# Optimization experiments

Measured on AMD Instinct MI355X. Metric: run time of the kernel, lower is better.

The kernel has to match this reference:

```python
import jax, jax.numpy as jnp
import numpy as np

DIM = 384
H = 64
W = 64
NB = 8
BS = DIM // NB
WF = W // 2 + 1
EPS = 1e-5


def _layernorm(x, g, b):
    mu = jnp.mean(x, axis=-1, keepdims=True)
    var = jnp.mean(jnp.square(x - mu), axis=-1, keepdims=True)
    return (x - mu) * jax.lax.rsqrt(var + EPS) * g + b


def setup_inputs() -> dict:
    key = jax.random.key(0)
    ks = jax.random.split(key, 8)
    scale = 0.02
    x = jax.random.normal(ks[0], (8, H, W, DIM), dtype=jnp.float32)
    # complex params stored as real view (..., 2) like torch.view_as_real
    w1 = scale * jax.random.normal(ks[1], (H, WF, NB, BS, BS, 2), dtype=jnp.float32)
    b1 = scale * jax.random.normal(ks[2], (H, WF, NB, BS, 2), dtype=jnp.float32)
    norm1_w = jnp.ones((DIM,), jnp.float32)
    norm1_b = jnp.zeros((DIM,), jnp.float32)
    norm2_w = jnp.ones((DIM,), jnp.float32)
    norm2_b = jnp.zeros((DIM,), jnp.float32)
    lim1 = 1.0 / np.sqrt(DIM)
    lim2 = 1.0 / np.sqrt(4 * DIM)
    mlp_w1 = jax.random.uniform(ks[3], (DIM, 4 * DIM), jnp.float32, -lim1, lim1)
    mlp_b1 = jax.random.uniform(ks[4], (4 * DIM,), jnp.float32, -lim1, lim1)
    mlp_w2 = jax.random.uniform(ks[5], (4 * DIM, DIM), jnp.float32, -lim2, lim2)
    mlp_b2 = jax.random.uniform(ks[6], (DIM,), jnp.float32, -lim2, lim2)
    return {"x": x, "w1": w1, "b1": b1, "norm1_w": norm1_w, "norm1_b": norm1_b,
            "norm2_w": norm2_w, "norm2_b": norm2_b, "mlp_w1": mlp_w1, "mlp_b1": mlp_b1,
            "mlp_w2": mlp_w2, "mlp_b2": mlp_b2}


def reference(x, w1, b1, norm1_w, norm1_b, norm2_w, norm2_b, mlp_w1, mlp_b1, mlp_w2, mlp_b2):
    B, h, w, C = x.shape
    residual = x
    xn = _layernorm(x, norm1_w, norm1_b)
    # spectral token mixing (fp32, ortho norm)
    xf = jnp.fft.rfft2(xn.astype(jnp.float32), axes=(1, 2), norm="ortho")  # (B,H,WF,C) complex
    xf = xf.reshape(B, h, w // 2 + 1, NB, BS)
    w1c = jax.lax.complex(w1[..., 0], w1[..., 1])  # (H,WF,NB,BS,BS)
    b1c = jax.lax.complex(b1[..., 0], b1[..., 1])  # (H,WF,NB,BS)
    o1 = jnp.einsum("bhwni,hwnio->bhwno", xf, w1c) + b1c
    o1 = jax.lax.complex(jax.nn.relu(o1.real), jax.nn.relu(o1.imag))
    o1 = o1.reshape(B, h, w // 2 + 1, C)
    xs = jnp.fft.irfft2(o1, s=(h, w), axes=(1, 2), norm="ortho")  # (B,H,W,C) real
    # channel MLP (dropout in eval mode = identity), exact GELU as torch default
    xm = _layernorm(xs, norm2_w, norm2_b)
    hdn = jax.nn.gelu(xm @ mlp_w1 + mlp_b1, approximate=False)
    mlp_out = hdn @ mlp_w2 + mlp_b2
    return xs + residual + mlp_out
```

## Files before the change

### kernel.cpp

```cpp
#include <hip/hip_runtime.h>
#include <math.h>


#define BB 8
#define CC 384
#define WF 33
#define NBK 8
#define BSZ 48
#define NTOK 32768
#define TW64 0.09817477042468103f

#define T_AWF 0
#define T_AHF 5120
#define T_AHI 21504
#define T_AWI 37888

typedef __attribute__((ext_vector_type(8))) short bf16x8;
typedef __attribute__((ext_vector_type(4))) float f32x4;

__device__ __forceinline__ unsigned short f2b(float f) {
  union { float f; unsigned u; } x; x.f = f;
  unsigned u = x.u;
  return (unsigned short)((u + 0x7fffu + ((u >> 16) & 1u)) >> 16);
}
__device__ __forceinline__ float b2fl(unsigned short u) {
  return __uint_as_float(((unsigned)u) << 16);
}
__device__ __forceinline__ void gload16(const void* g, void* l) {
  __builtin_amdgcn_global_load_lds(
      (const __attribute__((address_space(1))) void*)g,
      (__attribute__((address_space(3))) void*)l, 16, 0, 0);
}

__global__ __launch_bounds__(256) void prep_kernel(unsigned short* __restrict__ A,
    const float* __restrict__ mw1, unsigned short* __restrict__ w1t,
    const float* __restrict__ mw2, unsigned short* __restrict__ w2t,
    const float* __restrict__ n2w, const float* __restrict__ n2b,
    const float* __restrict__ mb1, float2* __restrict__ gsbb) {
  __shared__ float tile[32][33];
  int bid = blockIdx.x;
  if (bid < 64) {
    int idx0 = bid * 256 + threadIdx.x;
    const float S = 0.125f;
    for (int e = idx0; e < 5120; e += 16384) {
      int m = e >> 6, w = e & 63;
      float val = 0.f;
      if (m < 66) {
        int kwv = m >> 1;
        float th = (float)((kwv * w) & 63) * TW64;
        val = (m & 1) ? (((kwv==0)||(kwv==32)) ? 0.f : -sinf(th)*S) : cosf(th)*S;
      }
      A[T_AWF + e] = f2b(val);
    }
    for (int e = idx0; e < 16384; e += 16384) {
      int comp = e >> 13; int r = e & 8191; int mp = r >> 6, hh = r & 63;
      int cpo = mp >> 6, kh = mp & 63;
      float th = (float)((kh * hh) & 63) * TW64;
      float cv = cosf(th), sv = sinf(th);
      float fv = (cpo == 0) ? (comp == 0 ? cv : sv) : (comp == 0 ? -sv : cv);
      A[T_AHF + e] = f2b(fv * S);
      float iv = (cpo == 0) ? (comp == 0 ? cv : -sv) : (comp == 0 ? sv : cv);
      A[T_AHI + e] = f2b(iv * S);
    }
    for (int e = idx0; e < 4096; e += 16384) {
      int w = e >> 6, kp = e & 63;
      float val;
      if (kp <= 32) {
        float th = (float)((kp * w) & 63) * TW64;
        val = cosf(th) * (((kp==0)||(kp==32)) ? 1.f : 2.f) * S;
      } else {
        int k2 = kp - 32;
        float th = (float)((k2 * w) & 63) * TW64;
        val = -2.f * sinf(th) * S;
      }
      A[T_AWI + e] = f2b(val);
    }
    return;
  }
  if (bid >= 1216) {
    int n0 = (bid - 1216) * 256 + threadIdx.x;
    if (n0 < 1536) {
      float gsv = 0.f, bbv = 0.f;
      for (int k = 0; k < 384; ++k) {
        float a = mw1[(size_t)k*1536 + n0];
        gsv += n2w[k]*a;
        bbv += n2b[k]*a;
      }
      gsbb[n0] = make_float2(gsv, bbv + mb1[n0]);
    }
    return;
  }
  const float* in; unsigned short* outb; int R, C, tb; bool fold;
  if (bid < 640) { in = mw1; outb = w1t; R = 384; C = 1536; tb = bid - 64; fold = true; }
  else           { in = mw2; outb = w2t; R = 1536; C = 384; tb = bid - 640; fold = false; }
  int ntc = C >> 5;
  int bx = tb % ntc;
  int by = tb / ntc;
  int tx = threadIdx.x & 31, ty = threadIdx.x >> 5;
  for (int rr2 = ty; rr2 < 32; rr2 += 8)
    tile[rr2][tx] = in[(size_t)(by*32+rr2)*C + bx*32 + tx];
  __syncthreads();
  float gv = fold ? n2w[by*32 + tx] : 1.f;
  for (int rr2 = ty; rr2 < 32; rr2 += 8)
    outb[(size_t)(bx*32+rr2)*R + by*32 + tx] = f2b(tile[tx][rr2] * gv);
}

__global__ __launch_bounds__(256) void ln1t_kernel(const float* __restrict__ x,
    const float* __restrict__ g, const float* __restrict__ be,
    unsigned short* __restrict__ xn) {
  int outer = blockIdx.x;
  int tid = threadIdx.x, lane = tid & 63, wg = tid >> 6;
  const float* base = x + (size_t)outer * 64 * 384;
  float s[16], s2[16];
#pragma unroll
  for (int q = 0; q < 16; ++q) { s[q] = 0.f; s2[q] = 0.f; }
  for (int ch = 0; ch < 6; ++ch) {
#pragma unroll
    for (int q = 0; q < 16; ++q) {
      float v = base[(size_t)(wg*16 + q)*384 + ch*64 + lane];
      s[q] += v; s2[q] += v*v;
    }
  }
#pragma unroll
  for (int q = 0; q < 16; ++q) {
#pragma unroll
    for (int off = 32; off >= 1; off >>= 1) {
      s[q] += __shfl_xor(s[q], off);
      s2[q] += __shfl_xor(s2[q], off);
    }
  }
  float mu[16], rs[16];
#pragma unroll
  for (int q = 0; q < 16; ++q) {
    mu[q] = s[q] * (1.f/384.f);
    rs[q] = rsqrtf(s2[q] * (1.f/384.f) - mu[q]*mu[q] + 1e-5f);
  }
  unsigned short* o = xn + (size_t)outer * 384 * 64;
  for (int ch = 0; ch < 6; ++ch) {
    int c = ch*64 + lane;
    float ga = g[c], bb2 = be[c];
#pragma unroll
    for (int qq = 0; qq < 4; ++qq) {
      unsigned short hv[4];
#pragma unroll
      for (int r2 = 0; r2 < 4; ++r2) {
        int q = qq*4 + r2;
        hv[r2] = f2b((base[(size_t)(wg*16+q)*384 + c]-mu[q])*rs[q]*ga + bb2);
      }
      uint2 pw;
      pw.x = hv[0] | ((unsigned)hv[1] << 16);
      pw.y = hv[2] | ((unsigned)hv[3] << 16);
      *(uint2*)(o + (size_t)c*64 + wg*16 + qq*4) = pw;
    }
  }
}

template<int STAGE>
__global__ __launch_bounds__(256) void dft_kernel(
    const unsigned short* __restrict__ A0, const unsigned short* __restrict__ D,
    unsigned short* __restrict__ O) {
  constexpr int M = (STAGE==0) ? 80 : (STAGE==3) ? 64 : 128;
  constexpr int MT = M / 16;
  constexpr int NA = (STAGE==1 || STAGE==2) ? 2 : 1;
  constexpr int ABYTES = NA * M * 128;
  constexpr int STG = ABYTES + 16384;
  constexpr int EPB = 64 * 128 * 4;
  constexpr int SB = (STG > EPB) ? STG : EPB;
  __shared__ __align__(16) char smem[SB];
  char* BPL = smem + ABYTES;

  int bid = blockIdx.x;
  int cc = bid % 3; int outer = bid / 3;
  int c0 = cc * 128;
  int tid = threadIdx.x, lane = tid & 63, wid = tid >> 6;
  int rr = lane & 15, rq = lane >> 4;
  int b, h = 0, kw = 0;
  if (STAGE == 0 || STAGE == 3) { b = outer >> 6; h = outer & 63; }
  else { b = outer / 33; kw = outer % 33; }

  f32x4 acc[MT][2];
#pragma unroll
  for (int mt = 0; mt < MT; ++mt)
#pragma unroll
    for (int nt = 0; nt < 2; ++nt) acc[mt][nt] = (f32x4){0.f,0.f,0.f,0.f};

  const unsigned short* Atab =
    (STAGE==0) ? A0+T_AWF : (STAGE==1) ? A0+T_AHF : (STAGE==2) ? A0+T_AHI : A0+T_AWI;
  constexpr int ACH = NA * M * 8;
#pragma unroll
  for (int i = 0; i < (ACH + 255)/256; ++i) {
    int t2 = tid + i*256;
    if ((ACH % 256 == 0) || (t2 < ACH)) {
      int mm = t2 >> 3, ch = t2 & 7;
      gload16(Atab + mm*64 + ((ch ^ (mm & 7)) << 3), smem + i*4096 + wid*1024);
    }
  }

  int ncomp = (STAGE == 1) ? ((kw == 0 || kw == 32) ? 1 : 2) : NA;

  for (int comp = 0; comp < ncomp; ++comp) {
    if (comp) __syncthreads();
    if (STAGE == 0) {
      const unsigned short* src = D + (((size_t)(b*64 + h))*384 + c0) * 64;
#pragma unroll
      for (int i = 0; i < 4; ++i) {
        int idx = tid + i*256;
        int c = idx >> 3, ch = idx & 7;
        gload16(src + c*64 + ((ch ^ (c & 7)) << 3), BPL + i*4096 + wid*1024);
      }
    } else {
      size_t P; int RS;
      if (STAGE == 1) { P = (size_t)b*(64*66*384) + (size_t)(2*kw + comp)*384 + c0; RS = 66*384; }
      else if (STAGE == 2) { P = ((size_t)((b*2 + comp)*33) + kw)*64*384 + c0; RS = 384; }
      else { P = (size_t)b*(64*64*384) + (size_t)h*384 + c0; RS = 64*384; }
      const unsigned short* p0 = D + P;
#pragma unroll
      for (int i = 0; i < 4; ++i) {
        int kq = (tid >> 6) + i*4;
        int c2 = (tid & 63) * 2;
        const unsigned short* p = p0 + (size_t)(4*kq)*RS + c2;
        unsigned u0 = *(const unsigned*)p;
        unsigned u1 = *(const unsigned*)(p + RS);
        unsigned u2 = *(const unsigned*)(p + 2*(size_t)RS);
        unsigned u3 = *(const unsigned*)(p + 3*(size_t)RS);
        uint2 w0, w1v;
        w0.x = (u0 & 0xffffu) | (u1 << 16);
        w0.y = (u2 & 0xffffu) | (u3 << 16);
        w1v.x = (u0 >> 16) | (u1 & 0xffff0000u);
        w1v.y = (u2 >> 16) | (u3 & 0xffff0000u);
        *(uint2*)(BPL + c2*128 + ((kq*8) ^ ((c2 & 7) << 4))) = w0;
        *(uint2*)(BPL + (c2+1)*128 + ((kq*8) ^ (((c2+1) & 7) << 4))) = w1v;
      }
    }
    __syncthreads();
#pragma unroll
    for (int kh2 = 0; kh2 < 2; ++kh2) {
      int chb = kh2*4 + rq;
      bf16x8 bfr[2];
#pragma unroll
      for (int nt = 0; nt < 2; ++nt) {
        int n = wid*32 + nt*16 + rr;
        bfr[nt] = *(const bf16x8*)(BPL + n*128 + ((chb ^ (n & 7)) << 4));
      }
#pragma unroll
      for (int mt = 0; mt < MT; ++mt) {
        int mr = mt*16 + rr;
        bf16x8 af = *(const bf16x8*)(smem + comp*(M*128) + mr*128 + ((chb ^ (mr & 7)) << 4));
#pragma unroll
        for (int nt = 0; nt < 2; ++nt)
          acc[mt][nt] = __builtin_amdgcn_mfma_f32_16x16x32_bf16(af, bfr[nt], acc[mt][nt], 0, 0, 0);
      }
    }
  }
  __syncthreads();

  float* ep = (float*)smem;
  constexpr int NHM = (M + 63) / 64;
#pragma unroll
  for (int hm = 0; hm < NHM; ++hm) {
    if (hm) __syncthreads();
#pragma unroll
    for (int mo = 0; mo < 4; ++mo) {
      int mt = hm*4 + mo;
      if (mt >= MT) break;
#pragma unroll
      for (int nt = 0; nt < 2; ++nt)
#pragma unroll
        for (int j = 0; j < 4; ++j) {
          int m2 = mo*16 + rq*4 + j;
          int cl = wid*32 + nt*16 + rr;
          ep[m2*128 + (cl ^ ((m2 & 7) << 2))] = acc[mt][nt][j];
        }
    }
    __syncthreads();
    for (int it = tid; it < 64*16; it += 256) {
      int m2 = it >> 4, u8 = it & 15;
      int m = hm*64 + m2;
      if (m >= M) break;
      if (STAGE == 0 && m >= 66) break;
      if (STAGE == 2) { int cp = m >> 6; if (cp && (kw == 0 || kw == 32)) continue; }
      int swz = (m2 & 7) << 2;
      float4 v0 = *(const float4*)(ep + m2*128 + ((u8*8) ^ swz));
      float4 v1 = *(const float4*)(ep + m2*128 + ((u8*8 + 4) ^ swz));
      uint4 pw;
      pw.x = f2b(v0.x) | ((unsigned)f2b(v0.y) << 16);
      pw.y = f2b(v0.z) | ((unsigned)f2b(v0.w) << 16);
      pw.z = f2b(v1.x) | ((unsigned)f2b(v1.y) << 16);
      pw.w = f2b(v1.z) | ((unsigned)f2b(v1.w) << 16);
      size_t rowb;
      if (STAGE == 0) rowb = ((size_t)(b*64 + h)*66 + m)*384 + c0;
      else if (STAGE == 1) { int cp = m >> 6, kh = m & 63;
        rowb = (((size_t)((b*2 + cp)*64 + kh)*33) + kw)*384 + c0; }
      else if (STAGE == 2) { int cp = m >> 6, h2 = m & 63; int kp = cp ? 32 + kw : kw;
        rowb = ((size_t)(b*64 + kp)*64 + h2)*384 + c0; }
      else rowb = ((size_t)(b*64 + h)*64 + m)*384 + c0;
      *(uint4*)(O + rowb + u8*8) = pw;
    }
  }
}

__global__ __launch_bounds__(384) void blockmm2_kernel(
    const unsigned short* __restrict__ S2, const float* __restrict__ w1,
    const float* __restrict__ b1, unsigned short* __restrict__ o1) {
  int bid = blockIdx.x;
  int np = bid % 4;
  int kw = (bid / 4) % WF;
  int h = bid / (4*WF);
  int tid = threadIdx.x;
  __shared__ float4 wl4[2][48*24];
  __shared__ float2 xl[2][BB][48];
  __shared__ float2 bl[2][48];
#pragma unroll
  for (int e = tid; e < 2304; e += 384) {
    int sub = e / 1152, r = e % 1152;
    const float4* wb4 = (const float4*)(w1 + ((size_t)((h*WF + kw)*NBK) + 2*np + sub)*(BSZ*BSZ*2));
    wl4[sub][r] = wb4[r];
  }
  if (tid < 96) {
    int sub = tid / 48, o = tid % 48;
    bl[sub][o] = ((const float2*)b1)[((size_t)((h*WF + kw)*NBK) + 2*np + sub)*BSZ + o];
  }
#pragma unroll
  for (int e = tid; e < 768; e += 384) {
    int sub = e / 384, r = e % 384, bb = r / 48, i = r % 48;
    int n = 2*np + sub;
    size_t ir = (((size_t)((bb*2 + 0)*64 + h)*33) + kw)*384 + n*48 + i;
    size_t ii = (((size_t)((bb*2 + 1)*64 + h)*33) + kw)*384 + n*48 + i;
    xl[sub][bb][i] = make_float2(b2fl(S2[ir]), b2fl(S2[ii]));
  }
  __syncthreads();
  int sub = tid / 192, r = tid % 192, bb = r / 24, o2 = r % 24;
  float4 bv = *(const float4*)(&bl[sub][2*o2]);
  float2 a0 = make_float2(bv.x, bv.y);
  float2 a1 = make_float2(bv.z, bv.w);
#pragma unroll
  for (int i = 0; i < 48; ++i) {
    float2 xv = xl[sub][bb][i];
    float4 wv = wl4[sub][i*24 + o2];
    a0.x += xv.x*wv.x - xv.y*wv.y;
    a0.y += xv.x*wv.y + xv.y*wv.x;
    a1.x += xv.x*wv.z - xv.y*wv.w;
    a1.y += xv.x*wv.w + xv.y*wv.z;
  }
  int n = 2*np + sub;
  size_t idr = (((size_t)((bb*2 + 0)*33) + kw)*64 + h)*384 + n*48 + 2*o2;
  size_t idi = (((size_t)((bb*2 + 1)*33) + kw)*64 + h)*384 + n*48 + 2*o2;
  *(unsigned*)(o1 + idr) = f2b(fmaxf(a0.x, 0.f)) | ((unsigned)f2b(fmaxf(a1.x, 0.f)) << 16);
  *(unsigned*)(o1 + idi) = f2b(fmaxf(a0.y, 0.f)) | ((unsigned)f2b(fmaxf(a1.y, 0.f)) << 16);
}

__global__ __launch_bounds__(256) void stats_kernel(const unsigned short* __restrict__ in,
    float2* __restrict__ stats) {
  int token = blockIdx.x * 4 + (threadIdx.x >> 6);
  int lane = threadIdx.x & 63;
  const unsigned short* row = in + (size_t)token * CC;
  float s = 0.f, s2 = 0.f;
#pragma unroll
  for (int j = 0; j < 6; ++j) {
    float v = b2fl(row[lane + 64*j]);
    s += v; s2 += v*v;
  }
#pragma unroll
  for (int off = 32; off >= 1; off >>= 1) {
    s += __shfl_xor(s, off);
    s2 += __shfl_xor(s2, off);
  }
  if (lane == 0) {
    float mu = s * (1.0f/CC);
    float rs = rsqrtf(s2 * (1.0f/CC) - mu*mu + 1e-5f);
    stats[token] = make_float2(mu, rs);
  }
}

template<int MODE>
__global__ __launch_bounds__(256) void mfma_gemm_kernel(
    const unsigned short* __restrict__ A, int lda,
    const unsigned short* __restrict__ BT, int ldbt,
    void* __restrict__ Cp, int ldc, int K, int ntn,
    const float2* __restrict__ stats, const float2* __restrict__ gsbb,
    const unsigned short* __restrict__ xsb, const float* __restrict__ xres,
    const float* __restrict__ b2v) {
  __shared__ __align__(16) char gsm[32768];
  int nb = (int)gridDim.x;
  int bidx = (int)blockIdx.x;
  int bswz = (bidx & 7) * (nb >> 3) + (bidx >> 3);
  int bn = bswz % ntn;
  int bm = bswz / ntn;
  int t = threadIdx.x;
  int lane = t & 63;
  int wid = t >> 6;
  int wm = wid >> 1, wn = wid & 1;
  int rr = lane & 15, rq = lane >> 4;

  f32x4 acc[4][4];
#pragma unroll
  for (int m = 0; m < 4; ++m)
#pragma unroll
    for (int n = 0; n < 4; ++n) acc[m][n] = (f32x4){0.f,0.f,0.f,0.f};

  const unsigned short* Abase = A + (size_t)bm*128*lda;
  const unsigned short* Bbase = BT + (size_t)bn*128*ldbt;
  int nt = K >> 5;

#define STG(bsel, t0)                                                        \
  {                                                                          \
    _Pragma("unroll")                                                        \
    for (int i = 0; i < 2; ++i) {                                            \
      int u = t + i*256;                                                     \
      int row = u >> 2, ch = u & 3;                                          \
      gload16(Abase + (size_t)row*lda + (t0)*32 + ((ch ^ (row & 3)) << 3),   \
              gsm + (bsel)*16384 + i*4096 + wid*1024);                       \
      gload16(Bbase + (size_t)row*ldbt + (t0)*32 + ((ch ^ (row & 3)) << 3),  \
              gsm + (bsel)*16384 + 8192 + i*4096 + wid*1024);                \
    }                                                                        \
  }

#define CMP(bsel)                                                            \
  {                                                                          \
    const char* Ab2 = gsm + (bsel)*16384;                                    \
    const char* Bb2 = Ab2 + 8192;                                            \
    bf16x8 af[4], bfv[4];                                                    \
    _Pragma("unroll")                                                        \
    for (int m = 0; m < 4; ++m) {                                            \
      int row = wm*64 + m*16 + rr;                                           \
      af[m] = *(const bf16x8*)(Ab2 + row*64 + ((rq ^ (row & 3)) << 4));      \
    }                                                                        \
    _Pragma("unroll")                                                        \
    for (int n = 0; n < 4; ++n) {                                            \
      int row = wn*64 + n*16 + rr;                                           \
      bfv[n] = *(const bf16x8*)(Bb2 + row*64 + ((rq ^ (row & 3)) << 4));     \
    }                                                                        \
    _Pragma("unroll")                                                        \
    for (int m = 0; m < 4; ++m)                                              \
      _Pragma("unroll")                                                      \
      for (int n = 0; n < 4; ++n)                                            \
        acc[m][n] = __builtin_amdgcn_mfma_f32_16x16x32_bf16(af[m], bfv[n], acc[m][n], 0, 0, 0); \
  }

  STG(0, 0);
  __syncthreads();
  int cur = 0;
  for (int tt = 0; tt < nt - 1; ++tt) {
    STG(cur ^ 1, tt + 1);
    CMP(cur);
    __syncthreads();
    cur ^= 1;
  }
  CMP(cur);
  __syncthreads();

#undef STG
#undef CMP

  if (MODE == 0) {
    unsigned short* ep = (unsigned short*)gsm;
#pragma unroll
    for (int m = 0; m < 4; ++m) {
      float2 st[4];
#pragma unroll
      for (int j = 0; j < 4; ++j)
        st[j] = stats[bm*128 + wm*64 + m*16 + rq*4 + j];
#pragma unroll
      for (int n = 0; n < 4; ++n) {
        int lcol = wn*64 + n*16 + rr;
        float2 gb = gsbb[bn*128 + lcol];
#pragma unroll
        for (int j = 0; j < 4; ++j) {
          float v = st[j].y * acc[m][n][j] - st[j].y * st[j].x * gb.x + gb.y;
          v = 0.5f*v*(1.f + erff(v*0.70710678118654752f));
          int row = wm*64 + m*16 + rq*4 + j;
          ep[row*128 + (lcol ^ ((row & 7) << 3))] = f2b(v);
        }
      }
    }
    __syncthreads();
    for (int it = t; it < 128*16; it += 256) {
      int m = it >> 4, u8 = it & 15;
      uint4 pw = *(const uint4*)(ep + m*128 + ((u8*8) ^ ((m & 7) << 3)));
      *(uint4*)((unsigned short*)Cp + (size_t)(bm*128 + m)*ldc + bn*128 + u8*8) = pw;
    }
  } else {
    float* ep = (float*)gsm;
#pragma unroll
    for (int half = 0; half < 2; ++half) {
      __syncthreads();
#pragma unroll
      for (int mo = 0; mo < 2; ++mo) {
        int m = half*2 + mo;
#pragma unroll
        for (int n = 0; n < 4; ++n)
#pragma unroll
          for (int j = 0; j < 4; ++j) {
            int lr = wm*32 + mo*16 + rq*4 + j;
            int col = wn*64 + n*16 + rr;
            ep[lr*128 + (col ^ ((lr & 7) << 2))] = acc[m][n][j];
          }
      }
      __syncthreads();
      for (int it = t; it < 64*32; it += 256) {
        int lr = it >> 5, u = it & 31;
        int swz = (lr & 7) << 2;
        float4 v = *(const float4*)(ep + lr*128 + ((u*4) ^ swz));
        int grow = bm*128 + (lr >> 5)*64 + (half*2 + ((lr >> 4) & 1))*16 + (lr & 15);
        int gcol = bn*128 + u*4;
        size_t idx = (size_t)grow*ldc + gcol;
        float4 xr = *(const float4*)(xres + idx);
        uint2 xsv = *(const uint2*)(xsb + idx);
        float4 bv = *(const float4*)(b2v + gcol);
        float4 ov;
        ov.x = v.x + xr.x + b2fl((unsigned short)(xsv.x & 0xffffu)) + bv.x;
        ov.y = v.y + xr.y + b2fl((unsigned short)(xsv.x >> 16)) + bv.y;
        ov.z = v.z + xr.z + b2fl((unsigned short)(xsv.y & 0xffffu)) + bv.z;
        ov.w = v.w + xr.w + b2fl((unsigned short)(xsv.y >> 16)) + bv.w;
        *(float4*)((float*)Cp + idx) = ov;
      }
    }
  }
}

extern "C" void kernel_launch(void* const* d_in, const int* in_sizes, int n_in,
                              void* d_out, int out_size, void* d_ws, size_t ws_size,
                              hipStream_t stream) {
  const float* x   = (const float*)d_in[0];
  const float* w1  = (const float*)d_in[1];
  const float* b1  = (const float*)d_in[2];
  const float* n1w = (const float*)d_in[3];
  const float* n1b = (const float*)d_in[4];
  const float* n2w = (const float*)d_in[5];
  const float* n2b = (const float*)d_in[6];
  const float* mw1 = (const float*)d_in[7];
  const float* mb1 = (const float*)d_in[8];
  const float* mw2 = (const float*)d_in[9];
  const float* mb2 = (const float*)d_in[10];
  float* out = (float*)d_out;

  char* ws = (char*)d_ws;
  const size_t MB = 1ull << 20;
  unsigned short* xn  = (unsigned short*)(ws + 0*MB);
  unsigned short* S1  = (unsigned short*)(ws + 26*MB);
  unsigned short* S2  = (unsigned short*)(ws + 53*MB);
  unsigned short* o1  = (unsigned short*)(ws + 80*MB);
  unsigned short* S3  = (unsigned short*)(ws + 107*MB);
  unsigned short* xsb = (unsigned short*)(ws + 133*MB);
  float2*         stats = (float2*)(ws + 159*MB);
  unsigned short* hid = (unsigned short*)(ws + 185*MB);
  unsigned short* w1t = (unsigned short*)(ws + 286*MB);
  unsigned short* w2t = (unsigned short*)(ws + 288*MB);
  unsigned short* atab = (unsigned short*)(ws + 290*MB);
  float2*         gsbb = (float2*)(ws + 292*MB);

  prep_kernel<<<1222, 256, 0, stream>>>(atab, mw1, w1t, mw2, w2t, n2w, n2b, mb1, gsbb);

  ln1t_kernel<<<512, 256, 0, stream>>>(x, n1w, n1b, xn);
  dft_kernel<0><<<512*3, 256, 0, stream>>>(atab, xn, S1);
  dft_kernel<1><<<264*3, 256, 0, stream>>>(atab, S1, S2);
  blockmm2_kernel<<<64*WF*4, 384, 0, stream>>>(S2, w1, b1, o1);
  dft_kernel<2><<<264*3, 256, 0, stream>>>(atab, o1, S3);
  dft_kernel<3><<<512*3, 256, 0, stream>>>(atab, S3, xsb);
  stats_kernel<<<NTOK/4, 256, 0, stream>>>(xsb, stats);
  mfma_gemm_kernel<0><<<256*12, 256, 0, stream>>>(xsb, 384, w1t, 384,
                                                  hid, 1536, 384, 12,
                                                  stats, gsbb, nullptr, nullptr, nullptr);
  mfma_gemm_kernel<1><<<256*3, 256, 0, stream>>>(hid, 1536, w2t, 1536,
                                                 out, 384, 1536, 3,
                                                 nullptr, nullptr, xsb, x, mb2);
}
```

Measured before the change: 385.6 us.

## Fuse LN1 into first DFT, fold stats into DFT3, use FP8 for second MLP GEMM

Merges the LayerNorm1 transpose kernel into the first W-axis DFT so normalized tiles go straight to shared memory instead of through a global buffer. Per-token sum and sum-of-squares for LayerNorm2 are now computed in the last inverse DFT's epilogue as partial stats, which removes the separate stats kernel. The hidden activations and the second MLP weight are stored as scaled FP8 e4m3, and the second GEMM runs on fp8 MFMA with a rescale in the epilogue. This cuts memory traffic and kernel launches, but the lower precision on the second GEMM may hurt accuracy.

Measured after the change: 469.8 us. 21.8% more time.

```diff
diff --git a/kernel.cpp b/kernel.cpp
--- a/kernel.cpp
+++ b/kernel.cpp
@@ -26,6 +26,21 @@
 __device__ __forceinline__ float b2fl(unsigned short u) {
   return __uint_as_float(((unsigned)u) << 16);
 }
+__device__ __forceinline__ unsigned char f2e4m3(float f) {
+  unsigned u = __float_as_uint(f);
+  unsigned s = (u >> 24) & 0x80u;
+  float af = __uint_as_float(u & 0x7fffffffu);
+  if (af >= 464.f) return (unsigned char)(s | 0x7e);
+  if (af < 0.015625f) {
+    unsigned m = (unsigned)rintf(af * 512.f);
+    return (unsigned char)(s | m);
+  }
+  unsigned au = u & 0x7fffffffu;
+  au = au + 0x7ffffu + ((au >> 20) & 1u);
+  unsigned e32 = (au >> 23) - 127u;
+  unsigned mant = (au >> 20) & 7u;
+  return (unsigned char)(s | (((e32 + 7u) & 15u) << 3) | mant);
+}
 __device__ __forceinline__ void gload16(const void* g, void* l) {
   __builtin_amdgcn_global_load_lds(
       (const __attribute__((address_space(1))) void*)g,
@@ -34,7 +49,7 @@
 
 __global__ __launch_bounds__(256) void prep_kernel(unsigned short* __restrict__ A,
     const float* __restrict__ mw1, unsigned short* __restrict__ w1t,
-    const float* __restrict__ mw2, unsigned short* __restrict__ w2t,
+    const float* __restrict__ mw2, unsigned char* __restrict__ w2f8,
     const float* __restrict__ n2w, const float* __restrict__ n2b,
     const float* __restrict__ mb1, float2* __restrict__ gsbb) {
   __shared__ float tile[32][33];
@@ -90,67 +105,154 @@
     }
     return;
   }
-  const float* in; unsigned short* outb; int R, C, tb; bool fold;
-  if (bid < 640) { in = mw1; outb = w1t; R = 384; C = 1536; tb = bid - 64; fold = true; }
-  else           { in = mw2; outb = w2t; R = 1536; C = 384; tb = bid - 640; fold = false; }
-  int ntc = C >> 5;
-  int bx = tb % ntc;
-  int by = tb / ntc;
   int tx = threadIdx.x & 31, ty = threadIdx.x >> 5;
-  for (int rr2 = ty; rr2 < 32; rr2 += 8)
-    tile[rr2][tx] = in[(size_t)(by*32+rr2)*C + bx*32 + tx];
-  __syncthreads();
-  float gv = fold ? n2w[by*32 + tx] : 1.f;
-  for (int rr2 = ty; rr2 < 32; rr2 += 8)
-    outb[(size_t)(bx*32+rr2)*R + by*32 + tx] = f2b(tile[tx][rr2] * gv);
-}
-
-__global__ __launch_bounds__(256) void ln1t_kernel(const float* __restrict__ x,
+  if (bid < 640) {
+    int tb = bid - 64;
+    int ntc = 1536 >> 5;
+    int bx = tb % ntc, by = tb / ntc;
+    for (int rr2 = ty; rr2 < 32; rr2 += 8)
+      tile[rr2][tx] = mw1[(size_t)(by*32+rr2)*1536 + bx*32 + tx];
+    __syncthreads();
+    float gv = n2w[by*32 + tx];
+    for (int rr2 = ty; rr2 < 32; rr2 += 8)
+      w1t[(size_t)(bx*32+rr2)*384 + by*32 + tx] = f2b(tile[tx][rr2] * gv);
+  } else {
+    int tb = bid - 640;
+    int ntc = 384 >> 5;
+    int bx = tb % ntc, by = tb / ntc;
+    for (int rr2 = ty; rr2 < 32; rr2 += 8)
+      tile[rr2][tx] = mw2[(size_t)(by*32+rr2)*384 + bx*32 + tx];
+    __syncthreads();
+    for (int rr2 = ty; rr2 < 32; rr2 += 8)
+      w2f8[(size_t)(bx*32+rr2)*1536 + by*32 + tx] = f2e4m3(tile[tx][rr2] * 32.f);
+  }
+}
+
+__global__ __launch_bounds__(256) void ln1dft0_kernel(
+    const unsigned short* __restrict__ A0, const float* __restrict__ x,
     const float* __restrict__ g, const float* __restrict__ be,
-    unsigned short* __restrict__ xn) {
-  int outer = blockIdx.x;
-  int tid = threadIdx.x, lane = tid & 63, wg = tid >> 6;
+    unsigned short* __restrict__ S1) {
+  __shared__ __align__(16) char smem[32768];
+  char* BPL = smem + 10240;
+  float* stl = (float*)(smem + 26624);
+  int bid = blockIdx.x;
+  int cc = bid % 3; int outer = bid / 3;
+  int c0 = cc * 128;
+  int tid = threadIdx.x, lane = tid & 63, wid = tid >> 6;
+  int rr = lane & 15, rq = lane >> 4;
+  int b = outer >> 6, h = outer & 63;
+
+#pragma unroll
+  for (int i = 0; i < 3; ++i) {
+    int t2 = tid + i*256;
+    if (t2 < 640) {
+      int mm = t2 >> 3, ch = t2 & 7;
+      gload16(A0 + T_AWF + mm*64 + ((ch ^ (mm & 7)) << 3), smem + i*4096 + wid*1024);
+    }
+  }
   const float* base = x + (size_t)outer * 64 * 384;
-  float s[16], s2[16];
-#pragma unroll
-  for (int q = 0; q < 16; ++q) { s[q] = 0.f; s2[q] = 0.f; }
-  for (int ch = 0; ch < 6; ++ch) {
+  {
+    float s[16], s2[16];
+#pragma unroll
+    for (int q = 0; q < 16; ++q) { s[q] = 0.f; s2[q] = 0.f; }
+    for (int ch = 0; ch < 6; ++ch) {
+#pragma unroll
+      for (int q = 0; q < 16; ++q) {
+        float v = base[(size_t)(wid*16 + q)*384 + ch*64 + lane];
+        s[q] += v; s2[q] += v*v;
+      }
+    }
 #pragma unroll
     for (int q = 0; q < 16; ++q) {
-      float v = base[(size_t)(wg*16 + q)*384 + ch*64 + lane];
-      s[q] += v; s2[q] += v*v;
-    }
-  }
-#pragma unroll
-  for (int q = 0; q < 16; ++q) {
-#pragma unroll
-    for (int off = 32; off >= 1; off >>= 1) {
-      s[q] += __shfl_xor(s[q], off);
-      s2[q] += __shfl_xor(s2[q], off);
-    }
-  }
-  float mu[16], rs[16];
-#pragma unroll
-  for (int q = 0; q < 16; ++q) {
-    mu[q] = s[q] * (1.f/384.f);
-    rs[q] = rsqrtf(s2[q] * (1.f/384.f) - mu[q]*mu[q] + 1e-5f);
-  }
-  unsigned short* o = xn + (size_t)outer * 384 * 64;
-  for (int ch = 0; ch < 6; ++ch) {
-    int c = ch*64 + lane;
+#pragma unroll
+      for (int off = 32; off >= 1; off >>= 1) {
+        s[q] += __shfl_xor(s[q], off);
+        s2[q] += __shfl_xor(s2[q], off);
+      }
+      if (lane == q) {
+        float mu = s[q] * (1.f/384.f);
+        stl[2*(wid*16 + q)] = mu;
+        stl[2*(wid*16 + q) + 1] = rsqrtf(s2[q]*(1.f/384.f) - mu*mu + 1e-5f);
+      }
+    }
+  }
+  __syncthreads();
+#pragma unroll
+  for (int i = 0; i < 4; ++i) {
+    int task = tid + i*256;
+    int o = task >> 7, cl = task & 127;
+    int c = c0 + cl;
     float ga = g[c], bb2 = be[c];
-#pragma unroll
-    for (int qq = 0; qq < 4; ++qq) {
-      unsigned short hv[4];
-#pragma unroll
-      for (int r2 = 0; r2 < 4; ++r2) {
-        int q = qq*4 + r2;
-        hv[r2] = f2b((base[(size_t)(wg*16+q)*384 + c]-mu[q])*rs[q]*ga + bb2);
-      }
-      uint2 pw;
-      pw.x = hv[0] | ((unsigned)hv[1] << 16);
-      pw.y = hv[2] | ((unsigned)hv[3] << 16);
-      *(uint2*)(o + (size_t)c*64 + wg*16 + qq*4) = pw;
+    unsigned short hv[8];
+#pragma unroll
+    for (int k = 0; k < 8; ++k) {
+      int w = o*8 + k;
+      float v = base[(size_t)w*384 + c];
+      hv[k] = f2b((v - stl[2*w]) * stl[2*w+1] * ga + bb2);
+    }
+    uint4 pw;
+    pw.x = hv[0] | ((unsigned)hv[1] << 16);
+    pw.y = hv[2] | ((unsigned)hv[3] << 16);
+    pw.z = hv[4] | ((unsigned)hv[5] << 16);
+    pw.w = hv[6] | ((unsigned)hv[7] << 16);
+    *(uint4*)(BPL + cl*128 + ((o ^ (cl & 7)) << 4)) = pw;
+  }
+  __syncthreads();
+  f32x4 acc[5][2];
+#pragma unroll
+  for (int mt = 0; mt < 5; ++mt)
+#pragma unroll
+    for (int nt = 0; nt < 2; ++nt) acc[mt][nt] = (f32x4){0.f,0.f,0.f,0.f};
+#pragma unroll
+  for (int kh2 = 0; kh2 < 2; ++kh2) {
+    int chb = kh2*4 + rq;
+    bf16x8 bfr[2];
+#pragma unroll
+    for (int nt = 0; nt < 2; ++nt) {
+      int n = wid*32 + nt*16 + rr;
+      bfr[nt] = *(const bf16x8*)(BPL + n*128 + ((chb ^ (n & 7)) << 4));
+    }
+#pragma unroll
+    for (int mt = 0; mt < 5; ++mt) {
+      int mr = mt*16 + rr;
+      bf16x8 af = *(const bf16x8*)(smem + mr*128 + ((chb ^ (mr & 7)) << 4));
+#pragma unroll
+      for (int nt = 0; nt < 2; ++nt)
+        acc[mt][nt] = __builtin_amdgcn_mfma_f32_16x16x32_bf16(af, bfr[nt], acc[mt][nt], 0, 0, 0);
+    }
+  }
+  __syncthreads();
+  float* ep = (float*)smem;
+#pragma unroll
+  for (int hm = 0; hm < 2; ++hm) {
+    if (hm) __syncthreads();
+#pragma unroll
+    for (int mo = 0; mo < 4; ++mo) {
+      int mt = hm*4 + mo;
+      if (mt >= 5) break;
+#pragma unroll
+      for (int nt = 0; nt < 2; ++nt)
+#pragma unroll
+        for (int j = 0; j < 4; ++j) {
+          int m2 = mo*16 + rq*4 + j;
+          int cl = wid*32 + nt*16 + rr;
+          ep[m2*128 + (cl ^ ((m2 & 7) << 2))] = acc[mt][nt][j];
+        }
+    }
+    __syncthreads();
+    for (int it = tid; it < 64*16; it += 256) {
+      int m2 = it >> 4, u8 = it & 15;
+      int m = hm*64 + m2;
+      if (m >= 66) break;
+      int swz = (m2 & 7) << 2;
+      float4 v0 = *(const float4*)(ep + m2*128 + ((u8*8) ^ swz));
+      float4 v1 = *(const float4*)(ep + m2*128 + ((u8*8 + 4) ^ swz));
+      uint4 pw;
+      pw.x = f2b(v0.x) | ((unsigned)f2b(v0.y) << 16);
+      pw.y = f2b(v0.z) | ((unsigned)f2b(v0.w) << 16);
+      pw.z = f2b(v1.x) | ((unsigned)f2b(v1.y) << 16);
+      pw.w = f2b(v1.z) | ((unsigned)f2b(v1.w) << 16);
+      *(uint4*)(S1 + ((size_t)(b*64 + h)*66 + m)*384 + c0 + u8*8) = pw;
     }
   }
 }
@@ -158,14 +260,14 @@
 template<int STAGE>
 __global__ __launch_bounds__(256) void dft_kernel(
     const unsigned short* __restrict__ A0, const unsigned short* __restrict__ D,
-    unsigned short* __restrict__ O) {
-  constexpr int M = (STAGE==0) ? 80 : (STAGE==3) ? 64 : 128;
+    unsigned short* __restrict__ O, float2* __restrict__ statsp) {
+  constexpr int M = (STAGE==3) ? 64 : 128;
   constexpr int MT = M / 16;
   constexpr int NA = (STAGE==1 || STAGE==2) ? 2 : 1;
   constexpr int ABYTES = NA * M * 128;
-  constexpr int STG = ABYTES + 16384;
+  constexpr int STG2 = ABYTES + 16384;
   constexpr int EPB = 64 * 128 * 4;
-  constexpr int SB = (STG > EPB) ? STG : EPB;
+  constexpr int SB = (STG2 > EPB) ? STG2 : EPB;
   __shared__ __align__(16) char smem[SB];
   char* BPL = smem + ABYTES;
 
@@ -175,7 +277,7 @@
   int tid = threadIdx.x, lane = tid & 63, wid = tid >> 6;
   int rr = lane & 15, rq = lane >> 4;
   int b, h = 0, kw = 0;
-  if (STAGE == 0 || STAGE == 3) { b = outer >> 6; h = outer & 63; }
+  if (STAGE == 3) { b = outer >> 6; h = outer & 63; }
   else { b = outer / 33; kw = outer % 33; }
 
   f32x4 acc[MT][2];
@@ -185,7 +287,7 @@
     for (int nt = 0; nt < 2; ++nt) acc[mt][nt] = (f32x4){0.f,0.f,0.f,0.f};
 
   const unsigned short* Atab =
-    (STAGE==0) ? A0+T_AWF : (STAGE==1) ? A0+T_AHF : (STAGE==2) ? A0+T_AHI : A0+T_AWI;
+    (STAGE==1) ? A0+T_AHF : (STAGE==2) ? A0+T_AHI : A0+T_AWI;
   constexpr int ACH = NA * M * 8;
 #pragma unroll
   for (int i = 0; i < (ACH + 255)/256; ++i) {
@@ -200,37 +302,27 @@
 
   for (int comp = 0; comp < ncomp; ++comp) {
     if (comp) __syncthreads();
-    if (STAGE == 0) {
-      const unsigned short* src = D + (((size_t)(b*64 + h))*384 + c0) * 64;
-#pragma unroll
-      for (int i = 0; i < 4; ++i) {
-        int idx = tid + i*256;
-        int c = idx >> 3, ch = idx & 7;
-        gload16(src + c*64 + ((ch ^ (c & 7)) << 3), BPL + i*4096 + wid*1024);
-      }
-    } else {
-      size_t P; int RS;
-      if (STAGE == 1) { P = (size_t)b*(64*66*384) + (size_t)(2*kw + comp)*384 + c0; RS = 66*384; }
-      else if (STAGE == 2) { P = ((size_t)((b*2 + comp)*33) + kw)*64*384 + c0; RS = 384; }
-      else { P = (size_t)b*(64*64*384) + (size_t)h*384 + c0; RS = 64*384; }
-      const unsigned short* p0 = D + P;
-#pragma unroll
-      for (int i = 0; i < 4; ++i) {
-        int kq = (tid >> 6) + i*4;
-        int c2 = (tid & 63) * 2;
-        const unsigned short* p = p0 + (size_t)(4*kq)*RS + c2;
-        unsigned u0 = *(const unsigned*)p;
-        unsigned u1 = *(const unsigned*)(p + RS);
-        unsigned u2 = *(const unsigned*)(p + 2*(size_t)RS);
-        unsigned u3 = *(const unsigned*)(p + 3*(size_t)RS);
-        uint2 w0, w1v;
-        w0.x = (u0 & 0xffffu) | (u1 << 16);
-        w0.y = (u2 & 0xffffu) | (u3 << 16);
-        w1v.x = (u0 >> 16) | (u1 & 0xffff0000u);
-        w1v.y = (u2 >> 16) | (u3 & 0xffff0000u);
-        *(uint2*)(BPL + c2*128 + ((kq*8) ^ ((c2 & 7) << 4))) = w0;
-        *(uint2*)(BPL + (c2+1)*128 + ((kq*8) ^ (((c2+1) & 7) << 4))) = w1v;
-      }
+    size_t P; int RS;
+    if (STAGE == 1) { P = (size_t)b*(64*66*384) + (size_t)(2*kw + comp)*384 + c0; RS = 66*384; }
+    else if (STAGE == 2) { P = ((size_t)((b*2 + comp)*33) + kw)*64*384 + c0; RS = 384; }
+    else { P = (size_t)b*(64*64*384) + (size_t)h*384 + c0; RS = 64*384; }
+    const unsigned short* p0 = D + P;
+#pragma unroll
+    for (int i = 0; i < 4; ++i) {
+      int kq = (tid >> 6) + i*4;
+      int c2 = (tid & 63) * 2;
+      const unsigned short* p = p0 + (size_t)(4*kq)*RS + c2;
+      unsigned u0 = *(const unsigned*)p;
+      unsigned u1 = *(const unsigned*)(p + RS);
+      unsigned u2 = *(const unsigned*)(p + 2*(size_t)RS);
+      unsigned u3 = *(const unsigned*)(p + 3*(size_t)RS);
+      uint2 w0, w1v;
+      w0.x = (u0 & 0xffffu) | (u1 << 16);
+      w0.y = (u2 & 0xffffu) | (u3 << 16);
+      w1v.x = (u0 >> 16) | (u1 & 0xffff0000u);
+      w1v.y = (u2 >> 16) | (u3 & 0xffff0000u);
+      *(uint2*)(BPL + c2*128 + ((kq*8) ^ ((c2 & 7) << 4))) = w0;
+      *(uint2*)(BPL + (c2+1)*128 + ((kq*8) ^ (((c2+1) & 7) << 4))) = w1v;
     }
     __syncthreads();
 #pragma unroll
@@ -276,8 +368,6 @@
     for (int it = tid; it < 64*16; it += 256) {
       int m2 = it >> 4, u8 = it & 15;
       int m = hm*64 + m2;
-      if (m >= M) break;
-      if (STAGE == 0 && m >= 66) break;
       if (STAGE == 2) { int cp = m >> 6; if (cp && (kw == 0 || kw == 32)) continue; }
       int swz = (m2 & 7) << 2;
       float4 v0 = *(const float4*)(ep + m2*128 + ((u8*8) ^ swz));
@@ -288,14 +378,27 @@
       pw.z = f2b(v1.x) | ((unsigned)f2b(v1.y) << 16);
       pw.w = f2b(v1.z) | ((unsigned)f2b(v1.w) << 16);
       size_t rowb;
-      if (STAGE == 0) rowb = ((size_t)(b*64 + h)*66 + m)*384 + c0;
-      else if (STAGE == 1) { int cp = m >> 6, kh = m & 63;
+      if (STAGE == 1) { int cp = m >> 6, kh = m & 63;
         rowb = (((size_t)((b*2 + cp)*64 + kh)*33) + kw)*384 + c0; }
       else if (STAGE == 2) { int cp = m >> 6, h2 = m & 63; int kp = cp ? 32 + kw : kw;
         rowb = ((size_t)(b*64 + kp)*64 + h2)*384 + c0; }
       else rowb = ((size_t)(b*64 + h)*64 + m)*384 + c0;
       *(uint4*)(O + rowb + u8*8) = pw;
     }
+  }
+  if (STAGE == 3) {
+    int m = tid >> 2, qq = tid & 3;
+    float s = 0.f, s2 = 0.f;
+#pragma unroll
+    for (int u = 0; u < 32; ++u) {
+      int cl = qq*32 + u;
+      float v = ep[m*128 + (cl ^ ((m & 7) << 2))];
+      s += v; s2 += v*v;
+    }
+    s += __shfl_xor(s, 1); s += __shfl_xor(s, 2);
+    s2 += __shfl_xor(s2, 1); s2 += __shfl_xor(s2, 2);
+    if (qq == 0)
+      statsp[(size_t)cc*32768 + (size_t)(b*64 + h)*64 + m] = make_float2(s, s2);
   }
 }
 
@@ -349,43 +452,16 @@
   *(unsigned*)(o1 + idi) = f2b(fmaxf(a0.y, 0.f)) | ((unsigned)f2b(fmaxf(a1.y, 0.f)) << 16);
 }
 
-__global__ __launch_bounds__(256) void stats_kernel(const unsigned short* __restrict__ in,
-    float2* __restrict__ stats) {
-  int token = blockIdx.x * 4 + (threadIdx.x >> 6);
-  int lane = threadIdx.x & 63;
-  const unsigned short* row = in + (size_t)token * CC;
-  float s = 0.f, s2 = 0.f;
-#pragma unroll
-  for (int j = 0; j < 6; ++j) {
-    float v = b2fl(row[lane + 64*j]);
-    s += v; s2 += v*v;
-  }
-#pragma unroll
-  for (int off = 32; off >= 1; off >>= 1) {
-    s += __shfl_xor(s, off);
-    s2 += __shfl_xor(s2, off);
-  }
-  if (lane == 0) {
-    float mu = s * (1.0f/CC);
-    float rs = rsqrtf(s2 * (1.0f/CC) - mu*mu + 1e-5f);
-    stats[token] = make_float2(mu, rs);
-  }
-}
-
-template<int MODE>
-__global__ __launch_bounds__(256) void mfma_gemm_kernel(
-    const unsigned short* __restrict__ A, int lda,
-    const unsigned short* __restrict__ BT, int ldbt,
-    void* __restrict__ Cp, int ldc, int K, int ntn,
-    const float2* __restrict__ stats, const float2* __restrict__ gsbb,
-    const unsigned short* __restrict__ xsb, const float* __restrict__ xres,
-    const float* __restrict__ b2v) {
+__global__ __launch_bounds__(256) void gemm1_kernel(
+    const unsigned short* __restrict__ A, const unsigned short* __restrict__ BT,
+    unsigned char* __restrict__ hid, const float2* __restrict__ statsp,
+    const float2* __restrict__ gsbb) {
   __shared__ __align__(16) char gsm[32768];
   int nb = (int)gridDim.x;
   int bidx = (int)blockIdx.x;
   int bswz = (bidx & 7) * (nb >> 3) + (bidx >> 3);
-  int bn = bswz % ntn;
-  int bm = bswz / ntn;
+  int bn = bswz % 12;
+  int bm = bswz / 12;
   int t = threadIdx.x;
   int lane = t & 63;
   int wid = t >> 6;
@@ -398,9 +474,8 @@
 #pragma unroll
     for (int n = 0; n < 4; ++n) acc[m][n] = (f32x4){0.f,0.f,0.f,0.f};
 
-  const unsigned short* Abase = A + (size_t)bm*128*lda;
-  const unsigned short* Bbase = BT + (size_t)bn*128*ldbt;
-  int nt = K >> 5;
+  const unsigned short* Abase = A + (size_t)bm*128*384;
+  const unsigned short* Bbase = BT + (size_t)bn*128*384;
 
 #define STG(bsel, t0)                                                        \
   {                                                                          \
@@ -408,13 +483,12 @@
     for (int i = 0; i < 2; ++i) {                                            \
       int u = t + i*256;                                                     \
       int row = u >> 2, ch = u & 3;                                          \
-      gload16(Abase + (size_t)row*lda + (t0)*32 + ((ch ^ (row & 3)) << 3),   \
+      gload16(Abase + (size_t)row*384 + (t0)*32 + ((ch ^ (row & 3)) << 3),   \
               gsm + (bsel)*16384 + i*4096 + wid*1024);                       \
-      gload16(Bbase + (size_t)row*ldbt + (t0)*32 + ((ch ^ (row & 3)) << 3),  \
+      gload16(Bbase + (size_t)row*384 + (t0)*32 + ((ch ^ (row & 3)) << 3),   \
               gsm + (bsel)*16384 + 8192 + i*4096 + wid*1024);                \
     }                                                                        \
   }
-
 #define CMP(bsel)                                                            \
   {                                                                          \
     const char* Ab2 = gsm + (bsel)*16384;                                    \
@@ -440,7 +514,7 @@
   STG(0, 0);
   __syncthreads();
   int cur = 0;
-  for (int tt = 0; tt < nt - 1; ++tt) {
+  for (int tt = 0; tt < 11; ++tt) {
     STG(cur ^ 1, tt + 1);
     CMP(cur);
     __syncthreads();
@@ -448,72 +522,138 @@
   }
   CMP(cur);
   __syncthreads();
-
 #undef STG
 #undef CMP
 
-  if (MODE == 0) {
-    unsigned short* ep = (unsigned short*)gsm;
-#pragma unroll
-    for (int m = 0; m < 4; ++m) {
-      float2 st[4];
-#pragma unroll
-      for (int j = 0; j < 4; ++j)
-        st[j] = stats[bm*128 + wm*64 + m*16 + rq*4 + j];
+  unsigned char* ep = (unsigned char*)gsm;
+#pragma unroll
+  for (int m = 0; m < 4; ++m) {
+    float mu[4], rs[4];
+#pragma unroll
+    for (int j = 0; j < 4; ++j) {
+      int row = bm*128 + wm*64 + m*16 + rq*4 + j;
+      float2 p0 = statsp[row], p1 = statsp[32768 + row], p2 = statsp[65536 + row];
+      float sm = (p0.x + p1.x + p2.x) * (1.f/384.f);
+      float q2 = (p0.y + p1.y + p2.y) * (1.f/384.f);
+      mu[j] = sm;
+      rs[j] = rsqrtf(q2 - sm*sm + 1e-5f);
+    }
+#pragma unroll
+    for (int n = 0; n < 4; ++n) {
+      int lcol = wn*64 + n*16 + rr;
+      float2 gb = gsbb[bn*128 + lcol];
+#pragma unroll
+      for (int j = 0; j < 4; ++j) {
+        float v = rs[j] * acc[m][n][j] - rs[j] * mu[j] * gb.x + gb.y;
+        v = 0.5f*v*(1.f + erff(v*0.70710678118654752f));
+        int row = wm*64 + m*16 + rq*4 + j;
+        ep[row*128 + (lcol ^ ((row & 7) << 4))] = f2e4m3(v);
+      }
+    }
+  }
+  __syncthreads();
+  for (int it = t; it < 128*8; it += 256) {
+    int m = it >> 3, u16 = it & 7;
+    uint4 pw = *(const uint4*)(ep + m*128 + ((u16*16) ^ ((m & 7) << 4)));
+    *(uint4*)(hid + (size_t)(bm*128 + m)*1536 + bn*128 + u16*16) = pw;
+  }
+}
+
+__global__ __launch_bounds__(256) void gemm2_kernel(
+    const unsigned char* __restrict__ hid, const unsigned char* __restrict__ w2f8,
+    float* __restrict__ outp, const unsigned short* __restrict__ xsb,
+    const float* __restrict__ xres, const float* __restrict__ b2v) {
+  __shared__ __align__(16) char gsm[32768];
+  char* As = gsm;
+  char* Bs = gsm + 16384;
+  int nb = (int)gridDim.x;
+  int bidx = (int)blockIdx.x;
+  int bswz = (bidx & 7) * (nb >> 3) + (bidx >> 3);
+  int bn = bswz % 3;
+  int bm = bswz / 3;
+  int t = threadIdx.x;
+  int lane = t & 63;
+  int wid = t >> 6;
+  int wm = wid >> 1, wn = wid & 1;
+  int rr = lane & 15, rq = lane >> 4;
+
+  f32x4 acc[4][4];
+#pragma unroll
+  for (int m = 0; m < 4; ++m)
+#pragma unroll
+    for (int n = 0; n < 4; ++n) acc[m][n] = (f32x4){0.f,0.f,0.f,0.f};
+
+  const unsigned char* Abase = hid + (size_t)bm*128*1536;
+  const unsigned char* Bbase = w2f8 + (size_t)bn*128*1536;
+
+  for (int k0 = 0; k0 < 1536; k0 += 128) {
+#pragma unroll
+    for (int i = 0; i < 4; ++i) {
+      int idx = t + i*256;
+      int row = idx >> 3, ch = idx & 7;
+      gload16(Abase + (size_t)row*1536 + k0 + ((ch ^ (row & 7)) << 4),
+              As + i*4096 + wid*1024);
+      gload16(Bbase + (size_t)row*1536 + k0 + ((ch ^ (row & 7)) << 4),
+              Bs + i*4096 + wid*1024);
+    }
+    __syncthreads();
+#pragma unroll
+    for (int ks = 0; ks < 4; ++ks) {
+      int chunk = 2*ks + (rq >> 1);
+      int off8 = (rq & 1) << 3;
+      long long af[4], bf[4];
+#pragma unroll
+      for (int m = 0; m < 4; ++m) {
+        int row = wm*64 + m*16 + rr;
+        af[m] = *(const long long*)(As + row*128 + ((chunk ^ (row & 7)) << 4) + off8);
+      }
 #pragma unroll
       for (int n = 0; n < 4; ++n) {
-        int lcol = wn*64 + n*16 + rr;
-        float2 gb = gsbb[bn*128 + lcol];
+        int row = wn*64 + n*16 + rr;
+        bf[n] = *(const long long*)(Bs + row*128 + ((chunk ^ (row & 7)) << 4) + off8);
+      }
+#pragma unroll
+      for (int m = 0; m < 4; ++m)
+#pragma unroll
+        for (int n = 0; n < 4; ++n)
+          acc[m][n] = __builtin_amdgcn_mfma_f32_16x16x32_fp8_fp8(af[m], bf[n], acc[m][n], 0, 0, 0);
+    }
+    __syncthreads();
+  }
+
+  float* ep = (float*)gsm;
+#pragma unroll
+  for (int half = 0; half < 2; ++half) {
+    __syncthreads();
+#pragma unroll
+    for (int mo = 0; mo < 2; ++mo) {
+      int m = half*2 + mo;
+#pragma unroll
+      for (int n = 0; n < 4; ++n)
 #pragma unroll
         for (int j = 0; j < 4; ++j) {
-          float v = st[j].y * acc[m][n][j] - st[j].y * st[j].x * gb.x + gb.y;
-          v = 0.5f*v*(1.f + erff(v*0.70710678118654752f));
-          int row = wm*64 + m*16 + rq*4 + j;
-          ep[row*128 + (lcol ^ ((row & 7) << 3))] = f2b(v);
+          int lr = wm*32 + mo*16 + rq*4 + j;
+          int col = wn*64 + n*16 + rr;
+          ep[lr*128 + (col ^ ((lr & 7) << 2))] = acc[m][n][j];
         }
-      }
-    }
-    __syncthreads();
-    for (int it = t; it < 128*16; it += 256) {
-      int m = it >> 4, u8 = it & 15;
-      uint4 pw = *(const uint4*)(ep + m*128 + ((u8*8) ^ ((m & 7) << 3)));
-      *(uint4*)((unsigned short*)Cp + (size_t)(bm*128 + m)*ldc + bn*128 + u8*8) = pw;
-    }
-  } else {
-    float* ep = (float*)gsm;
-#pragma unroll
-    for (int half = 0; half < 2; ++half) {
-      __syncthreads();
-#pragma unroll
-      for (int mo = 0; mo < 2; ++mo) {
-        int m = half*2 + mo;
-#pragma unroll
-        for (int n = 0; n < 4; ++n)
-#pragma unroll
-          for (int j = 0; j < 4; ++j) {
-            int lr = wm*32 + mo*16 + rq*4 + j;
-            int col = wn*64 + n*16 + rr;
-            ep[lr*128 + (col ^ ((lr & 7) << 2))] = acc[m][n][j];
-          }
-      }
-      __syncthreads();
-      for (int it = t; it < 64*32; it += 256) {
-        int lr = it >> 5, u = it & 31;
-        int swz = (lr & 7) << 2;
-        float4 v = *(const float4*)(ep + lr*128 + ((u*4) ^ swz));
-        int grow = bm*128 + (lr >> 5)*64 + (half*2 + ((lr >> 4) & 1))*16 + (lr & 15);
-        int gcol = bn*128 + u*4;
-        size_t idx = (size_t)grow*ldc + gcol;
-        float4 xr = *(const float4*)(xres + idx);
-        uint2 xsv = *(const uint2*)(xsb + idx);
-        float4 bv = *(const float4*)(b2v + gcol);
-        float4 ov;
-        ov.x = v.x + xr.x + b2fl((unsigned short)(xsv.x & 0xffffu)) + bv.x;
-        ov.y = v.y + xr.y + b2fl((unsigned short)(xsv.x >> 16)) + bv.y;
-        ov.z = v.z + xr.z + b2fl((unsigned short)(xsv.y & 0xffffu)) + bv.z;
-        ov.w = v.w + xr.w + b2fl((unsigned short)(xsv.y >> 16)) + bv.w;
-        *(float4*)((float*)Cp + idx) = ov;
-      }
+    }
+    __syncthreads();
+    for (int it = t; it < 64*32; it += 256) {
+      int lr = it >> 5, u = it & 31;
+      int swz = (lr & 7) << 2;
+      float4 v = *(const float4*)(ep + lr*128 + ((u*4) ^ swz));
+      int grow = bm*128 + (lr >> 5)*64 + (half*2 + ((lr >> 4) & 1))*16 + (lr & 15);
+      int gcol = bn*128 + u*4;
+      size_t idx = (size_t)grow*384 + gcol;
+      float4 xr = *(const float4*)(xres + idx);
+      uint2 xsv = *(const uint2*)(xsb + idx);
+      float4 bv = *(const float4*)(b2v + gcol);
+      float4 ov;
+      ov.x = v.x*0.03125f + xr.x + b2fl((unsigned short)(xsv.x & 0xffffu)) + bv.x;
+      ov.y = v.y*0.03125f + xr.y + b2fl((unsigned short)(xsv.x >> 16)) + bv.y;
+      ov.z = v.z*0.03125f + xr.z + b2fl((unsigned short)(xsv.y & 0xffffu)) + bv.z;
+      ov.w = v.w*0.03125f + xr.w + b2fl((unsigned short)(xsv.y >> 16)) + bv.w;
+      *(float4*)(outp + idx) = ov;
     }
   }
 }
@@ -536,32 +676,24 @@
 
   char* ws = (char*)d_ws;
   const size_t MB = 1ull << 20;
-  unsigned short* xn  = (unsigned short*)(ws + 0*MB);
-  unsigned short* S1  = (unsigned short*)(ws + 26*MB);
-  unsigned short* S2  = (unsigned short*)(ws + 53*MB);
-  unsigned short* o1  = (unsigned short*)(ws + 80*MB);
-  unsigned short* S3  = (unsigned short*)(ws + 107*MB);
-  unsigned short* xsb = (unsigned short*)(ws + 133*MB);
-  float2*         stats = (float2*)(ws + 159*MB);
-  unsigned short* hid = (unsigned short*)(ws + 185*MB);
-  unsigned short* w1t = (unsigned short*)(ws + 286*MB);
-  unsigned short* w2t = (unsigned short*)(ws + 288*MB);
-  unsigned short* atab = (unsigned short*)(ws + 290*MB);
-  float2*         gsbb = (float2*)(ws + 292*MB);
-
-  prep_kernel<<<1222, 256, 0, stream>>>(atab, mw1, w1t, mw2, w2t, n2w, n2b, mb1, gsbb);
-
-  ln1t_kernel<<<512, 256, 0, stream>>>(x, n1w, n1b, xn);
-  dft_kernel<0><<<512*3, 256, 0, stream>>>(atab, xn, S1);
-  dft_kernel<1><<<264*3, 256, 0, stream>>>(atab, S1, S2);
+  unsigned short* S1  = (unsigned short*)(ws + 0*MB);
+  unsigned short* S2  = (unsigned short*)(ws + 27*MB);
+  unsigned short* o1  = (unsigned short*)(ws + 54*MB);
+  unsigned short* S3  = (unsigned short*)(ws + 81*MB);
+  unsigned short* xsb = (unsigned short*)(ws + 107*MB);
+  float2*         statsp = (float2*)(ws + 133*MB);
+  unsigned char*  hid = (unsigned char*)(ws + 134*MB);
+  unsigned short* w1t = (unsigned short*)(ws + 186*MB);
+  unsigned char*  w2f8 = (unsigned char*)(ws + 188*MB);
+  unsigned short* atab = (unsigned short*)(ws + 189*MB);
+  float2*         gsbb = (float2*)(ws + 190*MB);
+
+  prep_kernel<<<1222, 256, 0, stream>>>(atab, mw1, w1t, mw2, w2f8, n2w, n2b, mb1, gsbb);
+  ln1dft0_kernel<<<512*3, 256, 0, stream>>>(atab, x, n1w, n1b, S1);
+  dft_kernel<1><<<264*3, 256, 0, stream>>>(atab, S1, S2, nullptr);
   blockmm2_kernel<<<64*WF*4, 384, 0, stream>>>(S2, w1, b1, o1);
-  dft_kernel<2><<<264*3, 256, 0, stream>>>(atab, o1, S3);
-  dft_kernel<3><<<512*3, 256, 0, stream>>>(atab, S3, xsb);
-  stats_kernel<<<NTOK/4, 256, 0, stream>>>(xsb, stats);
-  mfma_gemm_kernel<0><<<256*12, 256, 0, stream>>>(xsb, 384, w1t, 384,
-                                                  hid, 1536, 384, 12,
-                                                  stats, gsbb, nullptr, nullptr, nullptr);
-  mfma_gemm_kernel<1><<<256*3, 256, 0, stream>>>(hid, 1536, w2t, 1536,
-                                                 out, 384, 1536, 3,
-                                                 nullptr, nullptr, xsb, x, mb2);
-}
+  dft_kernel<2><<<264*3, 256, 0, stream>>>(atab, o1, S3, nullptr);
+  dft_kernel<3><<<512*3, 256, 0, stream>>>(atab, S3, xsb, statsp);
+  gemm1_kernel<<<256*12, 256, 0, stream>>>(xsb, w1t, hid, (const float2*)statsp, gsbb);
+  gemm2_kernel<<<256*3, 256, 0, stream>>>(hid, w2f8, out, xsb, x, mb2);
+}
```
